# Kernel optimization log

Measured on AMD Instinct MI355X. Metric: run time of the kernel, lower is better.

The kernel has to match this reference:

```python
import jax, jax.numpy as jnp
import numpy as np

N_NODES = 100000
N_EDGES = 1200000
N_GRAPHS = 256
IN_C, HID_C, OUT_C = 5, 64, 2


def gcn_conv(x, src, dst, W, b, n_nodes):
    """PyG GCNConv: h = x@W; add self-loops; deg from target col (edge weight 1);
    norm = deg^{-1/2}[src]*deg^{-1/2}[dst]; scatter-add messages into dst; + bias."""
    loop = jnp.arange(n_nodes, dtype=src.dtype)
    s = jnp.concatenate([src, loop])
    d = jnp.concatenate([dst, loop])
    deg = jax.ops.segment_sum(jnp.ones_like(d, dtype=x.dtype), d, num_segments=n_nodes)
    dinv = jnp.where(deg > 0, jax.lax.rsqrt(deg), 0.0)
    norm = dinv[s] * dinv[d]                     # [E+N]
    h = x @ W                                    # [N, out]
    msg = h[s] * norm[:, None]                   # gather + scale  [E+N, out]
    out = jax.ops.segment_sum(msg, d, num_segments=n_nodes)  # scatter-add
    return out + b


def setup_inputs() -> dict:
    key = jax.random.key(0)
    ks = jax.random.split(key, 10)
    x = jax.random.normal(ks[0], (N_NODES, IN_C), dtype=jnp.float32)
    edge_index = jax.random.randint(ks[1], (2, N_EDGES), 0, N_NODES, dtype=jnp.int64)
    batch = jnp.sort(jax.random.randint(ks[2], (N_NODES,), 0, N_GRAPHS, dtype=jnp.int64))
    def glorot(k, fan_in, fan_out):
        lim = np.sqrt(6.0 / (fan_in + fan_out))
        return jax.random.uniform(k, (fan_in, fan_out), jnp.float32, -lim, lim)
    W1 = glorot(ks[3], IN_C, HID_C)
    b1 = jnp.zeros((HID_C,), jnp.float32)
    W2 = glorot(ks[4], HID_C, HID_C)
    b2 = jnp.zeros((HID_C,), jnp.float32)
    Wfc = glorot(ks[5], HID_C, OUT_C)
    bfc = jnp.zeros((OUT_C,), jnp.float32)
    return {"x": x, "edge_index": edge_index, "batch": batch,
            "W1": W1, "b1": b1, "W2": W2, "b2": b2, "Wfc": Wfc, "bfc": bfc}


def reference(x, edge_index, batch, W1, b1, W2, b2, Wfc, bfc):
    src, dst = edge_index[0], edge_index[1]
    h = jax.nn.relu(gcn_conv(x, src, dst, W1, b1, N_NODES))
    h = jax.nn.relu(gcn_conv(h, src, dst, W2, b2, N_NODES))
    # global_mean_pool over graph ids in `batch`
    sums = jax.ops.segment_sum(h, batch, num_segments=N_GRAPHS)          # [G, H]
    cnts = jax.ops.segment_sum(jnp.ones((h.shape[0],), h.dtype), batch,
                               num_segments=N_GRAPHS)                    # [G]
    pooled = sums / jnp.maximum(cnts, 1.0)[:, None]
    return pooled @ Wfc + bfc                                            # [G, 2]
```

## Files before the change

kernel.cpp:

```cpp
#include <hip/hip_runtime.h>

#define N_NODES 100000
#define N_EDGES 1200000
#define N_GRAPHS 256
#define IN_C 5
#define HID_C 64
#define OUT_C 2

#define BSH 7
#define BNODES 128
#define NB ((N_NODES + BNODES - 1) / BNODES)
#define CAPB 2048
#define EPB 2048
#define NCHUNK ((N_EDGES + EPB - 1) / EPB)
#define SEGS 784
#define GNPW 8
#define L1NPW 8

typedef unsigned int uint32;

__device__ __forceinline__ uint32 f2bf(float f) {
    uint32 x = __float_as_uint(f);
    return (x + 0x7FFFu + ((x >> 16) & 1u)) >> 16;
}
__device__ __forceinline__ float bflo(uint32 r) { return __uint_as_float(r << 16); }
__device__ __forceinline__ float bfhi(uint32 r) { return __uint_as_float(r & 0xFFFF0000u); }

__global__ void k_csort(const int* __restrict__ src, const int* __restrict__ dst,
                        int* __restrict__ pairs, int* __restrict__ seg,
                        float* __restrict__ pooled) {
    __shared__ int sp[EPB];
    __shared__ int hist[782];
    __shared__ int st[256];
    int c = blockIdx.x, t = threadIdx.x;
    if (c < (N_GRAPHS * HID_C) / 256)
        pooled[c * 256 + t] = 0.f;
    for (int i = t; i < 782; i += 256) hist[i] = 0;
    __syncthreads();
    int e0 = c * EPB;
    int n = N_EDGES - e0; if (n > EPB) n = EPB;
    int pk[8], bk[8];
#pragma unroll
    for (int i = 0; i < 8; ++i) {
        int idx = t + i * 256;
        if (idx < n) {
            int d = dst[e0 + idx];
            bk[i] = d >> BSH;
            pk[i] = ((d & (BNODES - 1)) << 17) | src[e0 + idx];
            atomicAdd(&hist[bk[i]], 1);
        } else bk[i] = -1;
    }
    __syncthreads();
    int i0 = t * 4;
    int v0 = (i0 + 0 < 782) ? hist[i0 + 0] : 0;
    int v1 = (i0 + 1 < 782) ? hist[i0 + 1] : 0;
    int v2 = (i0 + 2 < 782) ? hist[i0 + 2] : 0;
    int v3 = (i0 + 3 < 782) ? hist[i0 + 3] : 0;
    st[t] = v0 + v1 + v2 + v3;
    __syncthreads();
    for (int off = 1; off < 256; off <<= 1) {
        int a = (t >= off) ? st[t - off] : 0;
        __syncthreads();
        st[t] += a;
        __syncthreads();
    }
    int run = (t > 0) ? st[t - 1] : 0;
    if (i0 + 0 < 782) { hist[i0 + 0] = run; seg[c * SEGS + i0 + 0] = run; run += v0; }
    if (i0 + 1 < 782) { hist[i0 + 1] = run; seg[c * SEGS + i0 + 1] = run; run += v1; }
    if (i0 + 2 < 782) { hist[i0 + 2] = run; seg[c * SEGS + i0 + 2] = run; run += v2; }
    if (i0 + 3 < 782) { hist[i0 + 3] = run; seg[c * SEGS + i0 + 3] = run; run += v3; }
    if (t == 0) seg[c * SEGS + 782] = n;
    __syncthreads();
#pragma unroll
    for (int i = 0; i < 8; ++i)
        if (bk[i] >= 0) {
            int pos = atomicAdd(&hist[bk[i]], 1);
            sp[pos] = pk[i];
        }
    __syncthreads();
    for (int i = t; i < n; i += 256)
        pairs[c * EPB + i] = sp[i];
}

__global__ void k_bsort_xs(const int* __restrict__ pairs, const int* __restrict__ seg,
                           const float* __restrict__ x,
                           int* __restrict__ csr, int* __restrict__ rs,
                           int* __restrict__ cnt, float* __restrict__ dinv,
                           float* __restrict__ xs) {
    __shared__ int spairs[CAPB];
    __shared__ int ssorted[CAPB];
    __shared__ int ssrc[NCHUNK];
    __shared__ int sdst[NCHUNK];
    __shared__ int st[256];
    __shared__ int hist[BNODES];
    __shared__ int tmp[BNODES];
    __shared__ int cur[BNODES];
    __shared__ float sdv[BNODES];
    int b = blockIdx.x;
    int t = threadIdx.x;
    int base = b << BSH;
    for (int c = t; c < NCHUNK; c += 256) {
        int s0 = seg[c * SEGS + b];
        int s1 = seg[c * SEGS + b + 1];
        sdst[c] = s1 - s0;
        ssrc[c] = c * EPB + s0;
    }
    if (t < BNODES) hist[t] = 0;
    __syncthreads();
    int i0 = t * 4;
    int v0 = (i0 + 0 < NCHUNK) ? sdst[i0 + 0] : 0;
    int v1 = (i0 + 1 < NCHUNK) ? sdst[i0 + 1] : 0;
    int v2 = (i0 + 2 < NCHUNK) ? sdst[i0 + 2] : 0;
    int v3 = (i0 + 3 < NCHUNK) ? sdst[i0 + 3] : 0;
    st[t] = v0 + v1 + v2 + v3;
    __syncthreads();
    for (int off = 1; off < 256; off <<= 1) {
        int a = (t >= off) ? st[t - off] : 0;
        __syncthreads();
        st[t] += a;
        __syncthreads();
    }
    int run = (t > 0) ? st[t - 1] : 0;
    __syncthreads();
    if (i0 + 0 < NCHUNK) { sdst[i0 + 0] = run; run += v0; }
    if (i0 + 1 < NCHUNK) { sdst[i0 + 1] = run; run += v1; }
    if (i0 + 2 < NCHUNK) { sdst[i0 + 2] = run; run += v2; }
    if (i0 + 3 < NCHUNK) { sdst[i0 + 3] = run; run += v3; }
    __syncthreads();
    int n = st[255];
    if (n > CAPB) n = CAPB;
    for (int i = t; i < n; i += 256) {
        int lo = 0, hi = NCHUNK - 1;
        while (lo < hi) {
            int mid = (lo + hi + 1) >> 1;
            if (sdst[mid] <= i) lo = mid; else hi = mid - 1;
        }
        int p = pairs[ssrc[lo] + (i - sdst[lo])];
        spairs[i] = p;
        atomicAdd(&hist[p >> 17], 1);
    }
    __syncthreads();
    int v = (t < BNODES) ? hist[t] : 0;
    if (t < BNODES) tmp[t] = v;
    __syncthreads();
    for (int off = 1; off < BNODES; off <<= 1) {
        int a = (t < BNODES && t >= off) ? tmp[t - off] : 0;
        __syncthreads();
        if (t < BNODES) tmp[t] += a;
        __syncthreads();
    }
    float dv_t = rsqrtf((float)v + 1.0f);
    int s = b << 11;
    if (t < BNODES) {
        cur[t] = tmp[t] - v;
        sdv[t] = dv_t;
        if (base + t < N_NODES) {
            rs[base + t] = s + tmp[t] - v;
            cnt[base + t] = v;
            dinv[base + t] = dv_t;
        }
    }
    __syncthreads();
    for (int i = t; i < n; i += 256) {
        int p = spairs[i];
        int pos = atomicAdd(&cur[p >> 17], 1);
        ssorted[pos] = p & 0x1FFFF;
    }
    __syncthreads();
    for (int i = t; i < n; i += 256)
        csr[s + i] = ssorted[i];
    for (int i = t; i < BNODES * 8; i += 256) {
        int nl = i >> 3, k = i & 7;
        int node = base + nl;
        if (node < N_NODES && k < IN_C)
            xs[(unsigned)node * 8 + k] = x[(unsigned)node * IN_C + k] * sdv[nl];
    }
}

__global__ void __launch_bounds__(256) k_l1(
        const float* __restrict__ xs, const int* __restrict__ csr,
        const int* __restrict__ rs, const int* __restrict__ cnt,
        const float* __restrict__ dinv, const float* __restrict__ b1,
        const float* __restrict__ W1, const float* __restrict__ W2,
        uint32* __restrict__ g2t) {
    __shared__ __align__(16) float sagg[4][L1NPW][8];
    __shared__ __align__(16) float srow[4][2][HID_C];
    int tid = threadIdx.x;
    int w = tid >> 6;
    int lane = tid & 63;
    int base = (blockIdx.x * 4 + w) * L1NPW;

    int g = lane >> 3, l = lane & 7;
    int v = base + g;
    float a0 = 0.f, a1 = 0.f, a2 = 0.f, a3 = 0.f, a4 = 0.f;
    if (v < N_NODES) {
        int k0 = rs[v];
        int n = cnt[v];
        if (l == 0) {
            float4 p = *(const float4*)&xs[(unsigned)v * 8];
            a0 = p.x; a1 = p.y; a2 = p.z; a3 = p.w;
            a4 = xs[(unsigned)v * 8 + 4];
        }
        int i = l;
        int un = (i < n) ? csr[k0 + i] : -1;
        while (un >= 0) {
            int u = un;
            i += 8;
            un = (i < n) ? csr[k0 + i] : -1;
            float4 p = *(const float4*)&xs[(unsigned)u * 8];
            float p4 = xs[(unsigned)u * 8 + 4];
            a0 += p.x; a1 += p.y; a2 += p.z; a3 += p.w; a4 += p4;
        }
    }
#pragma unroll
    for (int off = 4; off; off >>= 1) {
        a0 += __shfl_xor(a0, off);
        a1 += __shfl_xor(a1, off);
        a2 += __shfl_xor(a2, off);
        a3 += __shfl_xor(a3, off);
        a4 += __shfl_xor(a4, off);
    }
    if (l == 0 && v < N_NODES) {
        *(float4*)&sagg[w][g][0] = make_float4(a0, a1, a2, a3);
        sagg[w][g][4] = a4;
    }

    int half = lane >> 5, c2 = lane & 31;
    int kb = half << 5;
    float2 w1r[IN_C];
#pragma unroll
    for (int k = 0; k < IN_C; ++k)
        w1r[k] = *(const float2*)&W1[k * HID_C + 2 * c2];
    float2 w2r[32];
#pragma unroll
    for (int j = 0; j < 32; ++j)
        w2r[j] = *(const float2*)&W2[(kb + j) * HID_C + 2 * c2];
    float2 bias = *(const float2*)&b1[2 * c2];

    for (int gg = 0; gg < L1NPW; ++gg) {
        int node = base + gg;
        if (node >= N_NODES) break;
        float dv = dinv[node];
        float4 qa = *(const float4*)&sagg[w][gg][0];
        float q4 = sagg[w][gg][4];
        float s0 = qa.x * w1r[0].x + qa.y * w1r[1].x + qa.z * w1r[2].x
                 + qa.w * w1r[3].x + q4 * w1r[4].x;
        float s1 = qa.x * w1r[0].y + qa.y * w1r[1].y + qa.z * w1r[2].y
                 + qa.w * w1r[3].y + q4 * w1r[4].y;
        float h0 = fmaxf(s0 * dv + bias.x, 0.f);
        float h1 = fmaxf(s1 * dv + bias.y, 0.f);
        int buf = gg & 1;
        if (half == 0) *(float2*)&srow[w][buf][2 * c2] = make_float2(h0, h1);
        float t0 = 0.f, t1 = 0.f;
#pragma unroll
        for (int jj = 0; jj < 8; ++jj) {
            float4 hv = *(const float4*)&srow[w][buf][kb + 4 * jj];
            t0 += hv.x * w2r[4 * jj + 0].x + hv.y * w2r[4 * jj + 1].x
                + hv.z * w2r[4 * jj + 2].x + hv.w * w2r[4 * jj + 3].x;
            t1 += hv.x * w2r[4 * jj + 0].y + hv.y * w2r[4 * jj + 1].y
                + hv.z * w2r[4 * jj + 2].y + hv.w * w2r[4 * jj + 3].y;
        }
        t0 += __shfl_xor(t0, 32);
        t1 += __shfl_xor(t1, 32);
        if (half == 0)
            g2t[(unsigned)node * 32 + c2] = (f2bf(t1 * dv) << 16) | f2bf(t0 * dv);
    }
}

#define LDU2(d, u) uint2 d = *(const uint2*)&g[(unsigned)(u) * 32 + 2 * c4]
#define ACC4(s0, s1, s2, s3, r) { s0 += bflo(r.x); s1 += bfhi(r.x); \
                                  s2 += bflo(r.y); s3 += bfhi(r.y); }
__global__ void __launch_bounds__(256, 4) k_gather2p(
        const uint32* __restrict__ g, const int* __restrict__ csr,
        const int* __restrict__ rs, const int* __restrict__ cnt,
        const float* __restrict__ dinv, const float* __restrict__ b,
        const int* __restrict__ batch, float* __restrict__ pooled) {
    int wv = __builtin_amdgcn_readfirstlane(
        blockIdx.x * (blockDim.x >> 6) + (threadIdx.x >> 6));
    int n0 = wv * GNPW;
    if (n0 >= N_NODES) return;
    int lane = threadIdx.x & 63;
    int sub = lane >> 4;
    int c4 = lane & 15;
    int va = n0 + sub, vb = n0 + 4 + sub;
    int ka = rs[va], na = cnt[va];
    int kb = rs[vb], nb = cnt[vb];
    float dva = dinv[va], dvb = dinv[vb];
    int ga = batch[va], gb = batch[vb];
    float4 bias = *(const float4*)&b[4 * c4];
    LDU2(rsa, va); LDU2(rsb, vb);
    float a0 = bflo(rsa.x), a1 = bfhi(rsa.x), a2 = bflo(rsa.y), a3 = bfhi(rsa.y);
    float y0 = bflo(rsb.x), y1 = bfhi(rsb.x), y2 = bflo(rsb.y), y3 = bfhi(rsb.y);
    int ia = 0, ib = 0;
    while (ia + 7 < na && ib + 7 < nb) {
        int u0 = csr[ka+ia+0], u1 = csr[ka+ia+1], u2 = csr[ka+ia+2], u3 = csr[ka+ia+3];
        int u4 = csr[ka+ia+4], u5 = csr[ka+ia+5], u6 = csr[ka+ia+6], u7 = csr[ka+ia+7];
        int w0 = csr[kb+ib+0], w1 = csr[kb+ib+1], w2 = csr[kb+ib+2], w3 = csr[kb+ib+3];
        int w4 = csr[kb+ib+4], w5 = csr[kb+ib+5], w6 = csr[kb+ib+6], w7 = csr[kb+ib+7];
        LDU2(p0, u0); LDU2(p1, u1); LDU2(p2, u2); LDU2(p3, u3);
        LDU2(p4, u4); LDU2(p5, u5); LDU2(p6, u6); LDU2(p7, u7);
        LDU2(q0, w0); LDU2(q1, w1); LDU2(q2, w2); LDU2(q3, w3);
        LDU2(q4, w4); LDU2(q5, w5); LDU2(q6, w6); LDU2(q7, w7);
        ACC4(a0, a1, a2, a3, p0); ACC4(a0, a1, a2, a3, p1);
        ACC4(a0, a1, a2, a3, p2); ACC4(a0, a1, a2, a3, p3);
        ACC4(a0, a1, a2, a3, p4); ACC4(a0, a1, a2, a3, p5);
        ACC4(a0, a1, a2, a3, p6); ACC4(a0, a1, a2, a3, p7);
        ACC4(y0, y1, y2, y3, q0); ACC4(y0, y1, y2, y3, q1);
        ACC4(y0, y1, y2, y3, q2); ACC4(y0, y1, y2, y3, q3);
        ACC4(y0, y1, y2, y3, q4); ACC4(y0, y1, y2, y3, q5);
        ACC4(y0, y1, y2, y3, q6); ACC4(y0, y1, y2, y3, q7);
        ia += 8; ib += 8;
    }
    while (ia + 7 < na) {
        int u0 = csr[ka+ia+0], u1 = csr[ka+ia+1], u2 = csr[ka+ia+2], u3 = csr[ka+ia+3];
        int u4 = csr[ka+ia+4], u5 = csr[ka+ia+5], u6 = csr[ka+ia+6], u7 = csr[ka+ia+7];
        LDU2(p0, u0); LDU2(p1, u1); LDU2(p2, u2); LDU2(p3, u3);
        LDU2(p4, u4); LDU2(p5, u5); LDU2(p6, u6); LDU2(p7, u7);
        ACC4(a0, a1, a2, a3, p0); ACC4(a0, a1, a2, a3, p1);
        ACC4(a0, a1, a2, a3, p2); ACC4(a0, a1, a2, a3, p3);
        ACC4(a0, a1, a2, a3, p4); ACC4(a0, a1, a2, a3, p5);
        ACC4(a0, a1, a2, a3, p6); ACC4(a0, a1, a2, a3, p7);
        ia += 8;
    }
    while (ib + 7 < nb) {
        int w0 = csr[kb+ib+0], w1 = csr[kb+ib+1], w2 = csr[kb+ib+2], w3 = csr[kb+ib+3];
        int w4 = csr[kb+ib+4], w5 = csr[kb+ib+5], w6 = csr[kb+ib+6], w7 = csr[kb+ib+7];
        LDU2(q0, w0); LDU2(q1, w1); LDU2(q2, w2); LDU2(q3, w3);
        LDU2(q4, w4); LDU2(q5, w5); LDU2(q6, w6); LDU2(q7, w7);
        ACC4(y0, y1, y2, y3, q0); ACC4(y0, y1, y2, y3, q1);
        ACC4(y0, y1, y2, y3, q2); ACC4(y0, y1, y2, y3, q3);
        ACC4(y0, y1, y2, y3, q4); ACC4(y0, y1, y2, y3, q5);
        ACC4(y0, y1, y2, y3, q6); ACC4(y0, y1, y2, y3, q7);
        ib += 8;
    }
    while (ia + 3 < na && ib + 3 < nb) {
        int u0 = csr[ka+ia+0], u1 = csr[ka+ia+1], u2 = csr[ka+ia+2], u3 = csr[ka+ia+3];
        int w0 = csr[kb+ib+0], w1 = csr[kb+ib+1], w2 = csr[kb+ib+2], w3 = csr[kb+ib+3];
        LDU2(p0, u0); LDU2(p1, u1); LDU2(p2, u2); LDU2(p3, u3);
        LDU2(q0, w0); LDU2(q1, w1); LDU2(q2, w2); LDU2(q3, w3);
        ACC4(a0, a1, a2, a3, p0); ACC4(a0, a1, a2, a3, p1);
        ACC4(a0, a1, a2, a3, p2); ACC4(a0, a1, a2, a3, p3);
        ACC4(y0, y1, y2, y3, q0); ACC4(y0, y1, y2, y3, q1);
        ACC4(y0, y1, y2, y3, q2); ACC4(y0, y1, y2, y3, q3);
        ia += 4; ib += 4;
    }
    while (ia + 3 < na) {
        int u0 = csr[ka+ia+0], u1 = csr[ka+ia+1], u2 = csr[ka+ia+2], u3 = csr[ka+ia+3];
        LDU2(p0, u0); LDU2(p1, u1); LDU2(p2, u2); LDU2(p3, u3);
        ACC4(a0, a1, a2, a3, p0); ACC4(a0, a1, a2, a3, p1);
        ACC4(a0, a1, a2, a3, p2); ACC4(a0, a1, a2, a3, p3);
        ia += 4;
    }
    while (ib + 3 < nb) {
        int w0 = csr[kb+ib+0], w1 = csr[kb+ib+1], w2 = csr[kb+ib+2], w3 = csr[kb+ib+3];
        LDU2(q0, w0); LDU2(q1, w1); LDU2(q2, w2); LDU2(q3, w3);
        ACC4(y0, y1, y2, y3, q0); ACC4(y0, y1, y2, y3, q1);
        ACC4(y0, y1, y2, y3, q2); ACC4(y0, y1, y2, y3, q3);
        ib += 4;
    }
    while (ia < na && ib < nb) {
        int u0 = csr[ka + ia], w0 = csr[kb + ib];
        LDU2(p0, u0); LDU2(q0, w0);
        ACC4(a0, a1, a2, a3, p0); ACC4(y0, y1, y2, y3, q0);
        ++ia; ++ib;
    }
    while (ia < na) {
        LDU2(p0, csr[ka + ia]);
        ACC4(a0, a1, a2, a3, p0);
        ++ia;
    }
    while (ib < nb) {
        LDU2(q0, csr[kb + ib]);
        ACC4(y0, y1, y2, y3, q0);
        ++ib;
    }
    float oa0 = fmaxf(a0 * dva + bias.x, 0.f);
    float oa1 = fmaxf(a1 * dva + bias.y, 0.f);
    float oa2 = fmaxf(a2 * dva + bias.z, 0.f);
    float oa3 = fmaxf(a3 * dva + bias.w, 0.f);
    float ob0 = fmaxf(y0 * dvb + bias.x, 0.f);
    float ob1 = fmaxf(y1 * dvb + bias.y, 0.f);
    float ob2 = fmaxf(y2 * dvb + bias.z, 0.f);
    float ob3 = fmaxf(y3 * dvb + bias.w, 0.f);
    int g0 = __builtin_amdgcn_readfirstlane(ga);
    if (__all(ga == g0) && __all(gb == g0)) {
        float f0 = oa0 + ob0, f1 = oa1 + ob1, f2 = oa2 + ob2, f3 = oa3 + ob3;
        f0 += __shfl_xor(f0, 16); f0 += __shfl_xor(f0, 32);
        f1 += __shfl_xor(f1, 16); f1 += __shfl_xor(f1, 32);
        f2 += __shfl_xor(f2, 16); f2 += __shfl_xor(f2, 32);
        f3 += __shfl_xor(f3, 16); f3 += __shfl_xor(f3, 32);
        if (sub == 0) {
            atomicAdd(&pooled[g0 * HID_C + 4 * c4 + 0], f0);
            atomicAdd(&pooled[g0 * HID_C + 4 * c4 + 1], f1);
            atomicAdd(&pooled[g0 * HID_C + 4 * c4 + 2], f2);
            atomicAdd(&pooled[g0 * HID_C + 4 * c4 + 3], f3);
        }
    } else {
        atomicAdd(&pooled[ga * HID_C + 4 * c4 + 0], oa0);
        atomicAdd(&pooled[ga * HID_C + 4 * c4 + 1], oa1);
        atomicAdd(&pooled[ga * HID_C + 4 * c4 + 2], oa2);
        atomicAdd(&pooled[ga * HID_C + 4 * c4 + 3], oa3);
        atomicAdd(&pooled[gb * HID_C + 4 * c4 + 0], ob0);
        atomicAdd(&pooled[gb * HID_C + 4 * c4 + 1], ob1);
        atomicAdd(&pooled[gb * HID_C + 4 * c4 + 2], ob2);
        atomicAdd(&pooled[gb * HID_C + 4 * c4 + 3], ob3);
    }
}

__global__ void k_fc(const float* __restrict__ pooled, const int* __restrict__ batch,
                     const float* __restrict__ Wfc, const float* __restrict__ bfc,
                     float* __restrict__ out) {
    int g = blockIdx.x;
    int c = threadIdx.x;
    int lo = 0, hi = N_NODES;
    while (lo < hi) { int mid = (lo + hi) >> 1; if (batch[mid] < g) lo = mid + 1; else hi = mid; }
    int start = lo;
    hi = N_NODES;
    while (lo < hi) { int mid = (lo + hi) >> 1; if (batch[mid] < g + 1) lo = mid + 1; else hi = mid; }
    int n = lo - start;
    float pv = pooled[g * HID_C + c] / (float)(n > 0 ? n : 1);
    float o0 = pv * Wfc[c * OUT_C + 0];
    float o1 = pv * Wfc[c * OUT_C + 1];
#pragma unroll
    for (int off = 32; off > 0; off >>= 1) {
        o0 += __shfl_down(o0, off);
        o1 += __shfl_down(o1, off);
    }
    if (c == 0) {
        out[g * OUT_C + 0] = o0 + bfc[0];
        out[g * OUT_C + 1] = o1 + bfc[1];
    }
}

extern "C" void kernel_launch(void* const* d_in, const int* in_sizes, int n_in,
                              void* d_out, int out_size, void* d_ws, size_t ws_size,
                              hipStream_t stream) {
    const float* x    = (const float*)d_in[0];
    const int*   ei   = (const int*)d_in[1];
    const int*   src  = ei;
    const int*   dst  = ei + N_EDGES;
    const int*   batch= (const int*)d_in[2];
    const float* W1   = (const float*)d_in[3];
    const float* b1   = (const float*)d_in[4];
    const float* W2   = (const float*)d_in[5];
    const float* b2   = (const float*)d_in[6];
    const float* Wfc  = (const float*)d_in[7];
    const float* bfc  = (const float*)d_in[8];
    float* out = (float*)d_out;

    float*  ws     = (float*)d_ws;
    float*  pooled = ws;
    float*  dinv   = ws + 16384;
    int*    cnt    = (int*)(dinv + 100352);
    int*    rs     = cnt + 100352;
    int*    seg    = rs + 100352;
    int*    pairs  = seg + NCHUNK * SEGS;
    int*    csr    = pairs + NCHUNK * EPB;
    float*  xs     = (float*)(csr + NB * CAPB);
    uint32* g2tab  = (uint32*)(xs + N_NODES * 8);

    k_csort<<<NCHUNK, 256, 0, stream>>>(src, dst, pairs, seg, pooled);
    k_bsort_xs<<<NB, 256, 0, stream>>>(pairs, seg, x, csr, rs, cnt, dinv, xs);

    {
        int blocks = (N_NODES + 4 * L1NPW - 1) / (4 * L1NPW);
        k_l1<<<blocks, 256, 0, stream>>>(xs, csr, rs, cnt, dinv, b1, W1, W2, g2tab);
    }

    {
        int waves = (N_NODES + GNPW - 1) / GNPW;
        int blocks = (waves + 3) / 4;
        k_gather2p<<<blocks, 256, 0, stream>>>(g2tab, csr, rs, cnt, dinv, b2, batch, pooled);
    }

    k_fc<<<N_GRAPHS, 64, 0, stream>>>(pooled, batch, Wfc, bfc, out);
}
```

Baseline: 188.1 us.

## Replace per-element binary search with max-scan segment lookup in bucket sort

The bucket-sort kernel now runs with 512 threads and finds the source chunk of each gathered edge with a marker array plus a max-prefix-scan, instead of a binary search per element over the chunk offsets. Each thread handles four consecutive slots and issues their global loads together. The aim is to cut the serial binary-search latency and dependent loads in the gather phase. In exchange it adds an extra shared array, a second 9-step scan with barriers, and larger blocks that may lower occupancy.

```diff
diff --git a/kernel.cpp b/kernel.cpp
--- a/kernel.cpp
+++ b/kernel.cpp
@@ -89,9 +89,10 @@
                            float* __restrict__ xs) {
     __shared__ int spairs[CAPB];
     __shared__ int ssorted[CAPB];
+    __shared__ int cid[CAPB];
     __shared__ int ssrc[NCHUNK];
     __shared__ int sdst[NCHUNK];
-    __shared__ int st[256];
+    __shared__ int st[512];
     __shared__ int hist[BNODES];
     __shared__ int tmp[BNODES];
     __shared__ int cur[BNODES];
@@ -99,46 +100,63 @@
     int b = blockIdx.x;
     int t = threadIdx.x;
     int base = b << BSH;
-    for (int c = t; c < NCHUNK; c += 256) {
+    for (int c = t; c < NCHUNK; c += 512) {
         int s0 = seg[c * SEGS + b];
         int s1 = seg[c * SEGS + b + 1];
         sdst[c] = s1 - s0;
         ssrc[c] = c * EPB + s0;
     }
+    for (int i = t; i < CAPB; i += 512) cid[i] = -1;
     if (t < BNODES) hist[t] = 0;
     __syncthreads();
-    int i0 = t * 4;
-    int v0 = (i0 + 0 < NCHUNK) ? sdst[i0 + 0] : 0;
+    int i0 = 2 * t;
+    int v0 = (i0 < NCHUNK) ? sdst[i0] : 0;
     int v1 = (i0 + 1 < NCHUNK) ? sdst[i0 + 1] : 0;
-    int v2 = (i0 + 2 < NCHUNK) ? sdst[i0 + 2] : 0;
-    int v3 = (i0 + 3 < NCHUNK) ? sdst[i0 + 3] : 0;
-    st[t] = v0 + v1 + v2 + v3;
-    __syncthreads();
-    for (int off = 1; off < 256; off <<= 1) {
+    st[t] = v0 + v1;
+    __syncthreads();
+    for (int off = 1; off < 512; off <<= 1) {
         int a = (t >= off) ? st[t - off] : 0;
         __syncthreads();
         st[t] += a;
         __syncthreads();
     }
     int run = (t > 0) ? st[t - 1] : 0;
-    __syncthreads();
-    if (i0 + 0 < NCHUNK) { sdst[i0 + 0] = run; run += v0; }
-    if (i0 + 1 < NCHUNK) { sdst[i0 + 1] = run; run += v1; }
-    if (i0 + 2 < NCHUNK) { sdst[i0 + 2] = run; run += v2; }
-    if (i0 + 3 < NCHUNK) { sdst[i0 + 3] = run; run += v3; }
-    __syncthreads();
-    int n = st[255];
+    int n = st[511];
     if (n > CAPB) n = CAPB;
-    for (int i = t; i < n; i += 256) {
-        int lo = 0, hi = NCHUNK - 1;
-        while (lo < hi) {
-            int mid = (lo + hi + 1) >> 1;
-            if (sdst[mid] <= i) lo = mid; else hi = mid - 1;
-        }
-        int p = pairs[ssrc[lo] + (i - sdst[lo])];
-        spairs[i] = p;
-        atomicAdd(&hist[p >> 17], 1);
-    }
+    __syncthreads();
+    int s0n = run, s1n = run + v0;
+    if (i0 < NCHUNK) sdst[i0] = s0n;
+    if (i0 + 1 < NCHUNK) sdst[i0 + 1] = s1n;
+    if (i0 < NCHUNK && v0 > 0 && s0n < CAPB) cid[s0n] = i0;
+    if (i0 + 1 < NCHUNK && v1 > 0 && s1n < CAPB) cid[s1n] = i0 + 1;
+    __syncthreads();
+    int sb = 4 * t;
+    int m0 = cid[sb];
+    int m1 = max(m0, cid[sb + 1]);
+    int m2 = max(m1, cid[sb + 2]);
+    int m3 = max(m2, cid[sb + 3]);
+    __syncthreads();
+    st[t] = m3;
+    __syncthreads();
+    for (int off = 1; off < 512; off <<= 1) {
+        int a = (t >= off) ? st[t - off] : -1;
+        __syncthreads();
+        st[t] = max(st[t], a);
+        __syncthreads();
+    }
+    int excl = (t > 0) ? st[t - 1] : -1;
+    int c0 = max(excl, m0), c1 = max(excl, m1);
+    int c2 = max(excl, m2), c3 = max(excl, m3);
+    int p0 = 0, p1 = 0, p2 = 0, p3 = 0;
+    int g0v = (sb + 0 < n), g1v = (sb + 1 < n), g2v = (sb + 2 < n), g3v = (sb + 3 < n);
+    if (g0v) p0 = pairs[ssrc[c0] + (sb + 0 - sdst[c0])];
+    if (g1v) p1 = pairs[ssrc[c1] + (sb + 1 - sdst[c1])];
+    if (g2v) p2 = pairs[ssrc[c2] + (sb + 2 - sdst[c2])];
+    if (g3v) p3 = pairs[ssrc[c3] + (sb + 3 - sdst[c3])];
+    if (g0v) { spairs[sb + 0] = p0; atomicAdd(&hist[p0 >> 17], 1); }
+    if (g1v) { spairs[sb + 1] = p1; atomicAdd(&hist[p1 >> 17], 1); }
+    if (g2v) { spairs[sb + 2] = p2; atomicAdd(&hist[p2 >> 17], 1); }
+    if (g3v) { spairs[sb + 3] = p3; atomicAdd(&hist[p3 >> 17], 1); }
     __syncthreads();
     int v = (t < BNODES) ? hist[t] : 0;
     if (t < BNODES) tmp[t] = v;
@@ -161,15 +179,15 @@
         }
     }
     __syncthreads();
-    for (int i = t; i < n; i += 256) {
+    for (int i = t; i < n; i += 512) {
         int p = spairs[i];
         int pos = atomicAdd(&cur[p >> 17], 1);
         ssorted[pos] = p & 0x1FFFF;
     }
     __syncthreads();
-    for (int i = t; i < n; i += 256)
+    for (int i = t; i < n; i += 512)
         csr[s + i] = ssorted[i];
-    for (int i = t; i < BNODES * 8; i += 256) {
+    for (int i = t; i < BNODES * 8; i += 512) {
         int nl = i >> 3, k = i & 7;
         int node = base + nl;
         if (node < N_NODES && k < IN_C)
@@ -460,7 +478,7 @@
     uint32* g2tab  = (uint32*)(xs + N_NODES * 8);
 
     k_csort<<<NCHUNK, 256, 0, stream>>>(src, dst, pairs, seg, pooled);
-    k_bsort_xs<<<NB, 256, 0, stream>>>(pairs, seg, x, csr, rs, cnt, dinv, xs);
+    k_bsort_xs<<<NB, 512, 0, stream>>>(pairs, seg, x, csr, rs, cnt, dinv, xs);
 
     {
         int blocks = (N_NODES + 4 * L1NPW - 1) / (4 * L1NPW);
```

After: 189.6 us. No clear change (+0.8%).
